# Kernel tuning notes

Measured on AMD Instinct MI355X. Metric: run time of the kernel, lower is better.

The kernel has to match this reference:

```python
import jax, jax.numpy as jnp
import numpy as np
from jax.ops import segment_sum

N_NODES = 100000


def _add_self_loops(edge_index, n):
    loop = jnp.arange(n, dtype=edge_index.dtype)
    src = jnp.concatenate([edge_index[0], loop])
    dst = jnp.concatenate([edge_index[1], loop])
    return src, dst


def _gcn_conv(x, W, b, src, dst, n):
    # PyG GCNConv: h = X W; out[i] = sum_j norm(j,i) h[j] + b, with self-loops
    h = x @ W                                             # [N, out]
    deg = segment_sum(jnp.ones_like(src, dtype=x.dtype), dst, num_segments=n)
    dinv = jnp.where(deg > 0, jax.lax.rsqrt(deg), 0.0)    # deg^{-1/2}
    norm = dinv[src] * dinv[dst]                          # [E]
    msg = h[src] * norm[:, None]                          # gather + scale
    out = segment_sum(msg, dst, num_segments=n)           # scatter-add
    return out + b


def setup_inputs() -> dict:
    key = jax.random.key(0)
    ks = jax.random.split(key, 8)
    x = jax.random.normal(ks[0], (N_NODES, 128), dtype=jnp.float32)
    edge_index = jax.random.randint(ks[1], (2, 600000), 0, N_NODES, dtype=jnp.int64)
    s1 = 1.0 / np.sqrt(128); s2 = 1.0 / np.sqrt(64); s3 = 1.0 / np.sqrt(32)
    return {
        "x": x,
        "edge_index": edge_index,
        "W1": jax.random.uniform(ks[2], (128, 64), jnp.float32, -s1, s1),
        "b1": jnp.zeros((64,), jnp.float32),
        "W2": jax.random.uniform(ks[3], (64, 32), jnp.float32, -s2, s2),
        "b2": jnp.zeros((32,), jnp.float32),
        "Wc": jax.random.uniform(ks[4], (32, 1), jnp.float32, -s3, s3),
        "bc": jnp.zeros((1,), jnp.float32),
    }


def reference(x, edge_index, W1, b1, W2, b2, Wc, bc):
    n = x.shape[0]
    src, dst = _add_self_loops(edge_index, n)
    h = jax.nn.relu(_gcn_conv(x, W1, b1, src, dst, n))
    h = jax.nn.relu(_gcn_conv(h, W2, b2, src, dst, n))
    return h @ Wc + bc
```

## Files before the change

### kernel.cpp

```cpp
#include <hip/hip_runtime.h>


#define SCAN_THREADS 256
#define SCAN_PER_T   8
#define SCAN_TILE    (SCAN_THREADS * SCAN_PER_T)

__global__ __launch_bounds__(256) void count_kernel(const int* __restrict__ dst,
                                                    int* __restrict__ deg, int E) {
    int e = blockIdx.x * blockDim.x + threadIdx.x;
    if (e < E) atomicAdd(&deg[dst[e]], 1);
}

__global__ __launch_bounds__(SCAN_THREADS) void tile_reduce_kernel(const int* __restrict__ deg,
                                                                   int* __restrict__ bsum,
                                                                   int n) {
    __shared__ int s[SCAN_THREADS];
    int t = threadIdx.x;
    int gbase = blockIdx.x * SCAN_TILE + t * SCAN_PER_T;
    int local = 0;
#pragma unroll
    for (int k = 0; k < SCAN_PER_T; ++k) {
        int i = gbase + k;
        if (i < n) local += deg[i];
    }
    s[t] = local;
    __syncthreads();
    for (int off = SCAN_THREADS / 2; off > 0; off >>= 1) {
        if (t < off) s[t] += s[t + off];
        __syncthreads();
    }
    if (t == 0) bsum[blockIdx.x] = s[0];
}

__global__ __launch_bounds__(SCAN_THREADS) void scan_bsums_kernel(int* __restrict__ bsum,
                                                                  int* __restrict__ row_ptr,
                                                                  int nb, int n) {
    __shared__ int s[SCAN_THREADS];
    int t = threadIdx.x;
    s[t] = (t < nb) ? bsum[t] : 0;
    __syncthreads();
    for (int off = 1; off < SCAN_THREADS; off <<= 1) {
        int v = (t >= off) ? s[t - off] : 0;
        __syncthreads();
        s[t] += v;
        __syncthreads();
    }
    if (t < nb) bsum[t] = (t == 0) ? 0 : s[t - 1];
    if (t == 0) row_ptr[n] = s[nb - 1];
}

__global__ __launch_bounds__(SCAN_THREADS) void tile_apply_kernel(int* __restrict__ deg,
                                                                  const int* __restrict__ bsum,
                                                                  int* __restrict__ row_ptr,
                                                                  float* __restrict__ dinv,
                                                                  int n) {
    __shared__ int s[SCAN_THREADS];
    int t = threadIdx.x;
    int gbase = blockIdx.x * SCAN_TILE + t * SCAN_PER_T;

    int d[SCAN_PER_T];
    int inc[SCAN_PER_T];
    int run = 0;
#pragma unroll
    for (int k = 0; k < SCAN_PER_T; ++k) {
        int i = gbase + k;
        d[k] = (i < n) ? deg[i] : 0;
        run += d[k];
        inc[k] = run;
    }
    s[t] = run;
    __syncthreads();
    for (int off = 1; off < SCAN_THREADS; off <<= 1) {
        int v = (t >= off) ? s[t - off] : 0;
        __syncthreads();
        s[t] += v;
        __syncthreads();
    }
    int base = bsum[blockIdx.x] + ((t == 0) ? 0 : s[t - 1]);
#pragma unroll
    for (int k = 0; k < SCAN_PER_T; ++k) {
        int i = gbase + k;
        if (i < n) {
            int ex = base + inc[k] - d[k];
            row_ptr[i] = ex;
            deg[i] = ex;
            dinv[i] = rsqrtf((float)(d[k] + 1));
        }
    }
}

__global__ __launch_bounds__(256) void fill_kernel(const int* __restrict__ src,
                                                   const int* __restrict__ dst,
                                                   int* __restrict__ cursor,
                                                   int* __restrict__ col, int E) {
    int e = blockIdx.x * blockDim.x + threadIdx.x;
    if (e < E) {
        int pos = atomicAdd(&cursor[dst[e]], 1);
        col[pos] = src[e];
    }
}

template <int IN, int OUT, int OSL, int BM, int TM, int TN>
__global__ __launch_bounds__(256) void gemm_tiled(const float* __restrict__ X,
                                                  const float* __restrict__ W,
                                                  const float* __restrict__ dinv,
                                                  float* __restrict__ H, int n) {
    constexpr int BK = 32;
    constexpr int S = 132;
    constexpr int NTX = OSL / TN;
    constexpr int NKT = IN / BK;
    static_assert(NTX * (BM / TM) == 256, "thread mapping");

    __shared__ float Ws[IN * OSL];
    __shared__ float Xs[2][BK * S];

    const int t = threadIdx.x;
    const int jb0 = blockIdx.y * OSL;
    for (int f = t; f < IN * OSL / 4; f += 256) {
        int row = f / (OSL / 4);
        int q = f % (OSL / 4);
        ((float4*)Ws)[f] = *(const float4*)(W + (size_t)row * OUT + jb0 + q * 4);
    }

    const int node0 = blockIdx.x * BM;
    const int tx = t % NTX;
    const int ty = t / NTX;
    const int row0 = ty * TM;
    const int jb = tx * TN;

    const int snd = t >> 3;
    const int skq = t & 7;

    float acc[TM][TN];
#pragma unroll
    for (int i = 0; i < TM; ++i)
#pragma unroll
        for (int j = 0; j < TN; ++j) acc[i][j] = 0.f;

    float4 stg[4];
#pragma unroll
    for (int i = 0; i < 4; ++i) {
        int nd = snd + 32 * i;
        stg[i] = make_float4(0.f, 0.f, 0.f, 0.f);
        if (node0 + nd < n)
            stg[i] = *(const float4*)(X + (size_t)(node0 + nd) * IN + skq * 4);
    }
#pragma unroll
    for (int i = 0; i < 4; ++i) {
        int nd = snd + 32 * i;
        float* p = Xs[0] + (skq * 4) * S + nd;
        p[0 * S] = stg[i].x; p[1 * S] = stg[i].y;
        p[2 * S] = stg[i].z; p[3 * S] = stg[i].w;
    }
    if (NKT > 1) {
#pragma unroll
        for (int i = 0; i < 4; ++i) {
            int nd = snd + 32 * i;
            stg[i] = make_float4(0.f, 0.f, 0.f, 0.f);
            if (node0 + nd < n)
                stg[i] = *(const float4*)(X + (size_t)(node0 + nd) * IN + BK + skq * 4);
        }
    }

    int cur = 0;
    for (int kt = 0; kt < NKT; ++kt) {
        __syncthreads();
        if (kt + 1 < NKT) {
#pragma unroll
            for (int i = 0; i < 4; ++i) {
                int nd = snd + 32 * i;
                float* p = Xs[cur ^ 1] + (skq * 4) * S + nd;
                p[0 * S] = stg[i].x; p[1 * S] = stg[i].y;
                p[2 * S] = stg[i].z; p[3 * S] = stg[i].w;
            }
        }
        if (kt + 2 < NKT) {
#pragma unroll
            for (int i = 0; i < 4; ++i) {
                int nd = snd + 32 * i;
                stg[i] = make_float4(0.f, 0.f, 0.f, 0.f);
                if (node0 + nd < n)
                    stg[i] = *(const float4*)(X + (size_t)(node0 + nd) * IN +
                                              (kt + 2) * BK + skq * 4);
            }
        }

        const float* xb = Xs[cur];
        const float* wb = Ws + (size_t)kt * BK * OSL + jb;
#pragma unroll 4
        for (int k = 0; k < BK; ++k) {
            float4 wv = *(const float4*)(wb + (size_t)k * OSL);
            float xv[TM];
#pragma unroll
            for (int i4 = 0; i4 < TM; i4 += 4) {
                float4 xq = *(const float4*)(xb + k * S + row0 + i4);
                xv[i4 + 0] = xq.x; xv[i4 + 1] = xq.y;
                xv[i4 + 2] = xq.z; xv[i4 + 3] = xq.w;
            }
#pragma unroll
            for (int i = 0; i < TM; ++i) {
                acc[i][0] += xv[i] * wv.x;
                acc[i][1] += xv[i] * wv.y;
                acc[i][2] += xv[i] * wv.z;
                acc[i][3] += xv[i] * wv.w;
            }
        }
        cur ^= 1;
    }

#pragma unroll
    for (int i = 0; i < TM; ++i) {
        int node = node0 + row0 + i;
        if (node < n) {
            float di = dinv[node];
            *(float4*)(H + (size_t)node * OUT + jb0 + jb) =
                make_float4(di * acc[i][0], di * acc[i][1],
                            di * acc[i][2], di * acc[i][3]);
        }
    }
}

template <int F>
__global__ __launch_bounds__(256) void agg_relu_kernel(const int* __restrict__ row_ptr,
                                                       const int* __restrict__ col,
                                                       const float* __restrict__ dinv,
                                                       const float* __restrict__ H,
                                                       const float* __restrict__ b,
                                                       float* __restrict__ OUT, int n) {
    constexpr int TPE = F / 4;
    int t = blockIdx.x * blockDim.x + threadIdx.x;
    int node = t / TPE;
    int c = t % TPE;
    if (node >= n) return;
    int rs = row_ptr[node], re = row_ptr[node + 1];
    float4 acc = make_float4(0.f, 0.f, 0.f, 0.f);
    int e = rs;
    for (; e + 3 < re; e += 4) {
        int s0 = col[e], s1 = col[e + 1], s2 = col[e + 2], s3 = col[e + 3];
        float4 v0 = *(const float4*)(H + (size_t)s0 * F + c * 4);
        float4 v1 = *(const float4*)(H + (size_t)s1 * F + c * 4);
        float4 v2 = *(const float4*)(H + (size_t)s2 * F + c * 4);
        float4 v3 = *(const float4*)(H + (size_t)s3 * F + c * 4);
        acc.x += (v0.x + v1.x) + (v2.x + v3.x);
        acc.y += (v0.y + v1.y) + (v2.y + v3.y);
        acc.z += (v0.z + v1.z) + (v2.z + v3.z);
        acc.w += (v0.w + v1.w) + (v2.w + v3.w);
    }
    for (; e < re; ++e) {
        int s0 = col[e];
        float4 v0 = *(const float4*)(H + (size_t)s0 * F + c * 4);
        acc.x += v0.x; acc.y += v0.y; acc.z += v0.z; acc.w += v0.w;
    }
    float di = dinv[node];
    float4 hs = *(const float4*)(H + (size_t)node * F + c * 4);
    float4 bb = *(const float4*)(b + c * 4);
    float4 r;
    r.x = di * (acc.x + hs.x) + bb.x;
    r.y = di * (acc.y + hs.y) + bb.y;
    r.z = di * (acc.z + hs.z) + bb.z;
    r.w = di * (acc.w + hs.w) + bb.w;
    r.x = r.x > 0.f ? r.x : 0.f;
    r.y = r.y > 0.f ? r.y : 0.f;
    r.z = r.z > 0.f ? r.z : 0.f;
    r.w = r.w > 0.f ? r.w : 0.f;
    *(float4*)(OUT + (size_t)node * F + c * 4) = r;
}

__global__ __launch_bounds__(256) void agg_final_kernel(const int* __restrict__ row_ptr,
                                                        const int* __restrict__ col,
                                                        const float* __restrict__ dinv,
                                                        const float* __restrict__ H,
                                                        const float* __restrict__ b2,
                                                        const float* __restrict__ Wc,
                                                        const float* __restrict__ bc,
                                                        float* __restrict__ out, int n) {
    constexpr int F = 32, TPE = 8;
    int t = blockIdx.x * blockDim.x + threadIdx.x;
    int node = t / TPE;
    int c = t % TPE;
    if (node >= n) return;
    int rs = row_ptr[node], re = row_ptr[node + 1];
    float4 acc = make_float4(0.f, 0.f, 0.f, 0.f);
    int e = rs;
    for (; e + 3 < re; e += 4) {
        int s0 = col[e], s1 = col[e + 1], s2 = col[e + 2], s3 = col[e + 3];
        float4 v0 = *(const float4*)(H + (size_t)s0 * F + c * 4);
        float4 v1 = *(const float4*)(H + (size_t)s1 * F + c * 4);
        float4 v2 = *(const float4*)(H + (size_t)s2 * F + c * 4);
        float4 v3 = *(const float4*)(H + (size_t)s3 * F + c * 4);
        acc.x += (v0.x + v1.x) + (v2.x + v3.x);
        acc.y += (v0.y + v1.y) + (v2.y + v3.y);
        acc.z += (v0.z + v1.z) + (v2.z + v3.z);
        acc.w += (v0.w + v1.w) + (v2.w + v3.w);
    }
    for (; e < re; ++e) {
        int s0 = col[e];
        float4 v0 = *(const float4*)(H + (size_t)s0 * F + c * 4);
        acc.x += v0.x; acc.y += v0.y; acc.z += v0.z; acc.w += v0.w;
    }
    float di = dinv[node];
    float4 hs = *(const float4*)(H + (size_t)node * F + c * 4);
    float4 bb = *(const float4*)(b2 + c * 4);
    float4 wc = *(const float4*)(Wc + c * 4);
    float4 r;
    r.x = di * (acc.x + hs.x) + bb.x;
    r.y = di * (acc.y + hs.y) + bb.y;
    r.z = di * (acc.z + hs.z) + bb.z;
    r.w = di * (acc.w + hs.w) + bb.w;
    float dot = (r.x > 0.f ? r.x : 0.f) * wc.x + (r.y > 0.f ? r.y : 0.f) * wc.y +
                (r.z > 0.f ? r.z : 0.f) * wc.z + (r.w > 0.f ? r.w : 0.f) * wc.w;
    dot += __shfl_xor(dot, 1, 8);
    dot += __shfl_xor(dot, 2, 8);
    dot += __shfl_xor(dot, 4, 8);
    if (c == 0) out[node] = dot + bc[0];
}

extern "C" void kernel_launch(void* const* d_in, const int* in_sizes, int n_in,
                              void* d_out, int out_size, void* d_ws, size_t ws_size,
                              hipStream_t stream) {
    const float* x  = (const float*)d_in[0];
    const int*   ei = (const int*)d_in[1];
    const float* W1 = (const float*)d_in[2];
    const float* b1 = (const float*)d_in[3];
    const float* W2 = (const float*)d_in[4];
    const float* b2 = (const float*)d_in[5];
    const float* Wc = (const float*)d_in[6];
    const float* bc = (const float*)d_in[7];
    float* out = (float*)d_out;

    const int n = in_sizes[0] / 128;
    const int E = in_sizes[1] / 2;

    const int* src = ei;
    const int* dst = ei + (size_t)E;

    const int nb = (n + SCAN_TILE - 1) / SCAN_TILE;

    float* dinv    = (float*)d_ws;
    int*   deg     = (int*)d_ws + n;
    int*   row_ptr = (int*)d_ws + 2 * (size_t)n;
    int*   col     = row_ptr + (n + 1);
    int*   bsum    = col + E;
    float* bufA    = (float*)(bsum + 256);
    float* bufB    = bufA + (size_t)n * 64;

    hipMemsetAsync(deg, 0, (size_t)n * 4, stream);
    count_kernel<<<(E + 255) / 256, 256, 0, stream>>>(dst, deg, E);
    tile_reduce_kernel<<<nb, SCAN_THREADS, 0, stream>>>(deg, bsum, n);
    scan_bsums_kernel<<<1, SCAN_THREADS, 0, stream>>>(bsum, row_ptr, nb, n);
    tile_apply_kernel<<<nb, SCAN_THREADS, 0, stream>>>(deg, bsum, row_ptr, dinv, n);
    fill_kernel<<<(E + 255) / 256, 256, 0, stream>>>(src, dst, deg, col, E);

    const int gemm_bx = (n + 127) / 128;

    {
        dim3 grid(gemm_bx, 2);
        gemm_tiled<128, 64, 32, 128, 4, 4><<<grid, 256, 0, stream>>>(x, W1, dinv, bufA, n);
    }
    agg_relu_kernel<64><<<(n * 16 + 255) / 256, 256, 0, stream>>>(row_ptr, col, dinv,
                                                                  bufA, b1, bufB, n);
    {
        dim3 grid(gemm_bx, 1);
        gemm_tiled<64, 32, 32, 128, 4, 4><<<grid, 256, 0, stream>>>(bufB, W2, dinv, bufA, n);
    }
    agg_final_kernel<<<(n * 8 + 255) / 256, 256, 0, stream>>>(row_ptr, col, dinv,
                                                              bufA, b2, Wc, bc, out, n);
}
```

Baseline: 266.5 us.

## Fuse layer-1 aggregation with layer-2 GEMM and widen first GEMM tile

The layer-1 aggregation+ReLU kernel now also performs the 64x32 layer-2 matrix multiply from shared memory, removing the intermediate 64-wide activation write/read and one kernel launch. The first GEMM computes all 64 output columns per block (TM=8) instead of splitting columns across two blocks, so each X tile is loaded from global memory only once. The tradeoffs are more registers per thread in the first GEMM and a block barrier plus a small dense GEMM step inside the gather-bound aggregation kernel.

Measured after the change: 258.4 us. 3.0% less time.

```diff
diff --git a/kernel.cpp b/kernel.cpp
--- a/kernel.cpp
+++ b/kernel.cpp
@@ -100,27 +100,23 @@
     }
 }
 
-template <int IN, int OUT, int OSL, int BM, int TM, int TN>
+template <int IN, int OUT, int BM, int TM, int TN>
 __global__ __launch_bounds__(256) void gemm_tiled(const float* __restrict__ X,
                                                   const float* __restrict__ W,
                                                   const float* __restrict__ dinv,
                                                   float* __restrict__ H, int n) {
     constexpr int BK = 32;
     constexpr int S = 132;
-    constexpr int NTX = OSL / TN;
+    constexpr int NTX = OUT / TN;
     constexpr int NKT = IN / BK;
     static_assert(NTX * (BM / TM) == 256, "thread mapping");
 
-    __shared__ float Ws[IN * OSL];
+    __shared__ float Ws[IN * OUT];
     __shared__ float Xs[2][BK * S];
 
     const int t = threadIdx.x;
-    const int jb0 = blockIdx.y * OSL;
-    for (int f = t; f < IN * OSL / 4; f += 256) {
-        int row = f / (OSL / 4);
-        int q = f % (OSL / 4);
-        ((float4*)Ws)[f] = *(const float4*)(W + (size_t)row * OUT + jb0 + q * 4);
-    }
+    for (int i = t; i < IN * OUT / 4; i += 256)
+        ((float4*)Ws)[i] = ((const float4*)W)[i];
 
     const int node0 = blockIdx.x * BM;
     const int tx = t % NTX;
@@ -186,10 +182,10 @@
         }
 
         const float* xb = Xs[cur];
-        const float* wb = Ws + (size_t)kt * BK * OSL + jb;
+        const float* wb = Ws + (size_t)kt * BK * OUT + jb;
 #pragma unroll 4
         for (int k = 0; k < BK; ++k) {
-            float4 wv = *(const float4*)(wb + (size_t)k * OSL);
+            float4 wv = *(const float4*)(wb + (size_t)k * OUT);
             float xv[TM];
 #pragma unroll
             for (int i4 = 0; i4 < TM; i4 += 4) {
@@ -213,57 +209,80 @@
         int node = node0 + row0 + i;
         if (node < n) {
             float di = dinv[node];
-            *(float4*)(H + (size_t)node * OUT + jb0 + jb) =
+            *(float4*)(H + (size_t)node * OUT + jb) =
                 make_float4(di * acc[i][0], di * acc[i][1],
                             di * acc[i][2], di * acc[i][3]);
         }
     }
 }
 
-template <int F>
-__global__ __launch_bounds__(256) void agg_relu_kernel(const int* __restrict__ row_ptr,
-                                                       const int* __restrict__ col,
-                                                       const float* __restrict__ dinv,
-                                                       const float* __restrict__ H,
-                                                       const float* __restrict__ b,
-                                                       float* __restrict__ OUT, int n) {
-    constexpr int TPE = F / 4;
-    int t = blockIdx.x * blockDim.x + threadIdx.x;
-    int node = t / TPE;
+__global__ __launch_bounds__(256) void agg_gemm2_kernel(const int* __restrict__ row_ptr,
+                                                        const int* __restrict__ col,
+                                                        const float* __restrict__ dinv,
+                                                        const float* __restrict__ H1,
+                                                        const float* __restrict__ b1,
+                                                        const float* __restrict__ W2,
+                                                        float* __restrict__ H2, int n) {
+    constexpr int F = 64, TPE = 16;
+    __shared__ float W2s[64 * 32];
+    __shared__ float hr[16][F + 4];
+
+    int t = threadIdx.x;
+    for (int i = t; i < 64 * 32 / 4; i += 256)
+        ((float4*)W2s)[i] = ((const float4*)W2)[i];
+
+    int ln = t / TPE;
     int c = t % TPE;
-    if (node >= n) return;
-    int rs = row_ptr[node], re = row_ptr[node + 1];
-    float4 acc = make_float4(0.f, 0.f, 0.f, 0.f);
-    int e = rs;
-    for (; e + 3 < re; e += 4) {
-        int s0 = col[e], s1 = col[e + 1], s2 = col[e + 2], s3 = col[e + 3];
-        float4 v0 = *(const float4*)(H + (size_t)s0 * F + c * 4);
-        float4 v1 = *(const float4*)(H + (size_t)s1 * F + c * 4);
-        float4 v2 = *(const float4*)(H + (size_t)s2 * F + c * 4);
-        float4 v3 = *(const float4*)(H + (size_t)s3 * F + c * 4);
-        acc.x += (v0.x + v1.x) + (v2.x + v3.x);
-        acc.y += (v0.y + v1.y) + (v2.y + v3.y);
-        acc.z += (v0.z + v1.z) + (v2.z + v3.z);
-        acc.w += (v0.w + v1.w) + (v2.w + v3.w);
-    }
-    for (; e < re; ++e) {
-        int s0 = col[e];
-        float4 v0 = *(const float4*)(H + (size_t)s0 * F + c * 4);
-        acc.x += v0.x; acc.y += v0.y; acc.z += v0.z; acc.w += v0.w;
-    }
-    float di = dinv[node];
-    float4 hs = *(const float4*)(H + (size_t)node * F + c * 4);
-    float4 bb = *(const float4*)(b + c * 4);
-    float4 r;
-    r.x = di * (acc.x + hs.x) + bb.x;
-    r.y = di * (acc.y + hs.y) + bb.y;
-    r.z = di * (acc.z + hs.z) + bb.z;
-    r.w = di * (acc.w + hs.w) + bb.w;
-    r.x = r.x > 0.f ? r.x : 0.f;
-    r.y = r.y > 0.f ? r.y : 0.f;
-    r.z = r.z > 0.f ? r.z : 0.f;
-    r.w = r.w > 0.f ? r.w : 0.f;
-    *(float4*)(OUT + (size_t)node * F + c * 4) = r;
+    int node = blockIdx.x * 16 + ln;
+    float di = 0.f;
+
+    if (node < n) {
+        int rs = row_ptr[node], re = row_ptr[node + 1];
+        float4 acc = make_float4(0.f, 0.f, 0.f, 0.f);
+        int e = rs;
+        for (; e + 3 < re; e += 4) {
+            int s0 = col[e], s1 = col[e + 1], s2 = col[e + 2], s3 = col[e + 3];
+            float4 v0 = *(const float4*)(H1 + (size_t)s0 * F + c * 4);
+            float4 v1 = *(const float4*)(H1 + (size_t)s1 * F + c * 4);
+            float4 v2 = *(const float4*)(H1 + (size_t)s2 * F + c * 4);
+            float4 v3 = *(const float4*)(H1 + (size_t)s3 * F + c * 4);
+            acc.x += (v0.x + v1.x) + (v2.x + v3.x);
+            acc.y += (v0.y + v1.y) + (v2.y + v3.y);
+            acc.z += (v0.z + v1.z) + (v2.z + v3.z);
+            acc.w += (v0.w + v1.w) + (v2.w + v3.w);
+        }
+        for (; e < re; ++e) {
+            int s0 = col[e];
+            float4 v0 = *(const float4*)(H1 + (size_t)s0 * F + c * 4);
+            acc.x += v0.x; acc.y += v0.y; acc.z += v0.z; acc.w += v0.w;
+        }
+        di = dinv[node];
+        float4 hs = *(const float4*)(H1 + (size_t)node * F + c * 4);
+        float4 bb = *(const float4*)(b1 + c * 4);
+        float rx = di * (acc.x + hs.x) + bb.x;
+        float ry = di * (acc.y + hs.y) + bb.y;
+        float rz = di * (acc.z + hs.z) + bb.z;
+        float rw = di * (acc.w + hs.w) + bb.w;
+        hr[ln][c * 4 + 0] = rx > 0.f ? rx : 0.f;
+        hr[ln][c * 4 + 1] = ry > 0.f ? ry : 0.f;
+        hr[ln][c * 4 + 2] = rz > 0.f ? rz : 0.f;
+        hr[ln][c * 4 + 3] = rw > 0.f ? rw : 0.f;
+    }
+    __syncthreads();
+
+    if (node < n) {
+        int j = c * 2;
+        float s0 = 0.f, s1 = 0.f;
+        const float* hrow = hr[ln];
+#pragma unroll 8
+        for (int k = 0; k < 64; ++k) {
+            float h = hrow[k];
+            s0 += h * W2s[k * 32 + j];
+            s1 += h * W2s[k * 32 + j + 1];
+        }
+        H2[(size_t)node * 32 + j]     = di * s0;
+        H2[(size_t)node * 32 + j + 1] = di * s1;
+    }
 }
 
 __global__ __launch_bounds__(256) void agg_final_kernel(const int* __restrict__ row_ptr,
@@ -353,16 +372,11 @@
 
     const int gemm_bx = (n + 127) / 128;
 
-    {
-        dim3 grid(gemm_bx, 2);
-        gemm_tiled<128, 64, 32, 128, 4, 4><<<grid, 256, 0, stream>>>(x, W1, dinv, bufA, n);
-    }
-    agg_relu_kernel<64><<<(n * 16 + 255) / 256, 256, 0, stream>>>(row_ptr, col, dinv,
-                                                                  bufA, b1, bufB, n);
-    {
-        dim3 grid(gemm_bx, 1);
-        gemm_tiled<64, 32, 32, 128, 4, 4><<<grid, 256, 0, stream>>>(bufB, W2, dinv, bufA, n);
-    }
+    gemm_tiled<128, 64, 128, 8, 4><<<gemm_bx, 256, 0, stream>>>(x, W1, dinv, bufA, n);
+
+    agg_gemm2_kernel<<<(n + 15) / 16, 256, 0, stream>>>(row_ptr, col, dinv,
+                                                        bufA, b1, W2, bufB, n);
+
     agg_final_kernel<<<(n * 8 + 255) / 256, 256, 0, stream>>>(row_ptr, col, dinv,
-                                                              bufA, b2, Wc, bc, out, n);
-}
+                                                              bufB, b2, Wc, bc, out, n);
+}
```
